# Kernel optimization log

Measured on AMD Instinct MI355X. Metric: run time of the kernel, lower is better.

Reference implementation:

```python
import jax, jax.numpy as jnp
import numpy as np

NUM_ROUTING_ITER = 3

def _squash(x):
    # Faithful to torch x.norm(): GLOBAL Frobenius norm over the whole tensor.
    n2 = jnp.sum(x * x)
    return x * (jnp.sqrt(n2) / (1.0 + n2))

def setup_inputs() -> dict:
    key = jax.random.key(0)
    k1, k2 = jax.random.split(key)
    x = jax.random.normal(k1, (256, 1152, 8), dtype=jnp.float32)
    weight = jax.random.normal(k2, (10, 1152, 8, 16), dtype=jnp.float32)
    return {"x": x, "weight": weight}

def reference(x, weight):
    # priors: [NC, B, IC, 1, OC] from [1,B,IC,1,L] @ [NC,1,IC,L,OC]
    priors = jnp.einsum('bil,nilo->nbio', x, weight)[:, :, :, None, :]
    b = jnp.zeros_like(priors)
    v = None
    for _ in range(NUM_ROUTING_ITER):
        # legacy F.softmax with no dim on a 5D tensor -> dim=1 (batch dim)
        c = jax.nn.softmax(b, axis=1)
        s = jnp.sum(c * priors, axis=2, keepdims=True)  # [NC,B,1,1,OC]
        v = _squash(s)
        b = b + jnp.sum(priors * v, axis=-1, keepdims=True)
    return v
```

## Files before the change

kernel.cpp:

```cpp
#include <hip/hip_runtime.h>
#include <math.h>

#define NC    10
#define BATCH 256
#define IC    1152
#define LDIM  8
#define OC    16

#define NCH   96
#define CH    (IC/NCH)
#define NBLK  (NC*NCH)
#define NTHR  256
#define NTOT  (NC*BATCH*OC)
#define NRED  160
#define KPG   (NCH/4)

typedef float f32x2 __attribute__((ext_vector_type(2)));

__device__ __forceinline__ void decode_nch(int bid, int& n, int& ch) {
    n = bid / NCH;
    int r = bid - n * NCH;
    ch = (r & 7) * (NCH / 8) + (r >> 3);
}

__device__ __forceinline__ float n2_reduce(const float* __restrict__ n2_part,
                                           float* redW, int t, int lane, int wid)
{
    float q = (t < NRED) ? n2_part[t] : 0.f;
#pragma unroll
    for (int m = 32; m >= 1; m >>= 1) q += __shfl_xor(q, m, 64);
    if (lane == 0) redW[wid] = q;
    __syncthreads();
    return redW[0] + redW[1] + redW[2] + redW[3];
}

__global__ __launch_bounds__(256) void k0_xT(const float* __restrict__ x,
                                             float* __restrict__ xT)
{
    int u = blockIdx.x * 256 + threadIdx.x;
    int i = u >> 9, r = u & 511, b = r >> 1, h = r & 1;
    reinterpret_cast<float4*>(xT)[u] =
        reinterpret_cast<const float4*>(x)[((size_t)b * IC + i) * 2 + h];
}

__global__ __launch_bounds__(256) void kA(
    const float* __restrict__ xT, const float* __restrict__ w,
    float* __restrict__ s_part)
{
    int n, ch; decode_nch(blockIdx.x, n, ch);
    int i0 = ch * CH;
    int t  = threadIdx.x;

    f32x2 sp2[8];
#pragma unroll
    for (int j = 0; j < 8; ++j) sp2[j] = (f32x2){0.f, 0.f};

    for (int ii = 0; ii < CH; ++ii) {
        int i = i0 + ii;
        const float4* xp = reinterpret_cast<const float4*>(xT)
                         + ((size_t)i * BATCH + t) * 2;
        float4 xa = xp[0], xb = xp[1];
        float xr[8] = {xa.x, xa.y, xa.z, xa.w, xb.x, xb.y, xb.z, xb.w};
        const f32x2* wp2 = reinterpret_cast<const f32x2*>(
            w + (size_t)__builtin_amdgcn_readfirstlane((n * IC + i) * (LDIM * OC)));
#pragma unroll
        for (int l = 0; l < LDIM; ++l) {
            f32x2 xl = {xr[l], xr[l]};
#pragma unroll
            for (int j = 0; j < 8; ++j)
                sp2[j] += wp2[l * 8 + j] * xl;
        }
    }
    float4* dst = reinterpret_cast<float4*>(s_part)
                + (((size_t)ch * NC + n) * BATCH + t) * 4;
    const float inv = 1.0f / 256.0f;
    dst[0] = make_float4(sp2[0].x*inv, sp2[0].y*inv, sp2[1].x*inv, sp2[1].y*inv);
    dst[1] = make_float4(sp2[2].x*inv, sp2[2].y*inv, sp2[3].x*inv, sp2[3].y*inv);
    dst[2] = make_float4(sp2[4].x*inv, sp2[4].y*inv, sp2[5].x*inv, sp2[5].y*inv);
    dst[3] = make_float4(sp2[6].x*inv, sp2[6].y*inv, sp2[7].x*inv, sp2[7].y*inv);
}

__global__ __launch_bounds__(256) void kR(const float* __restrict__ s_part,
                                          float* __restrict__ s,
                                          float* __restrict__ n2_part)
{
    __shared__ float4 lds[4][64];
    int t = threadIdx.x, lane = t & 63, g = t >> 6;
    int idx0 = blockIdx.x * 256;
    float4 a = make_float4(0.f, 0.f, 0.f, 0.f);
    for (int k = 0; k < KPG; ++k) {
        float4 v = *reinterpret_cast<const float4*>(
            s_part + (size_t)(g * KPG + k) * NTOT + idx0 + lane * 4);
        a.x += v.x; a.y += v.y; a.z += v.z; a.w += v.w;
    }
    lds[g][lane] = a;
    __syncthreads();
    if (t < 64) {
        float4 s0 = lds[0][t], s1 = lds[1][t], s2 = lds[2][t], s3 = lds[3][t];
        float4 sv = make_float4(s0.x+s1.x+s2.x+s3.x, s0.y+s1.y+s2.y+s3.y,
                                s0.z+s1.z+s2.z+s3.z, s0.w+s1.w+s2.w+s3.w);
        *reinterpret_cast<float4*>(s + idx0 + t * 4) = sv;
        float q = sv.x*sv.x + sv.y*sv.y + sv.z*sv.z + sv.w*sv.w;
#pragma unroll
        for (int m = 32; m >= 1; m >>= 1) q += __shfl_xor(q, m, 64);
        if (t == 0) n2_part[blockIdx.x] = q;
    }
}

template<bool FIRST>
__global__ __launch_bounds__(256) void kB(
    const float* __restrict__ xT, const float* __restrict__ w,
    const float* __restrict__ s, const float* __restrict__ n2_part,
    float* __restrict__ betaT, float* __restrict__ s_part)
{
    __shared__ float redA[2][4];
    __shared__ float redW[4];
    int t = threadIdx.x, lane = t & 63, wid = t >> 6;
    int n, ch; decode_nch(blockIdx.x, n, ch);
    int i0 = ch * CH;

    float n2 = n2_reduce(n2_part, redW, t, lane, wid);
    float sc = sqrtf(n2) / (1.0f + n2);

    f32x2 v2[8];
    {
        const f32x2* svp = reinterpret_cast<const f32x2*>(s)
                         + ((size_t)n * BATCH + t) * 8;
        f32x2 scv = {sc, sc};
#pragma unroll
        for (int j = 0; j < 8; ++j) v2[j] = svp[j] * scv;
    }

    f32x2 sp2[8];
#pragma unroll
    for (int j = 0; j < 8; ++j) sp2[j] = (f32x2){0.f, 0.f};

    const float4* xbase = reinterpret_cast<const float4*>(xT);
    size_t xo = ((size_t)i0 * BATCH + t) * 2;
    float4 xa = xbase[xo], xb = xbase[xo + 1];

    for (int ii = 0; ii < CH; ++ii) {
        int i = i0 + ii;
        float4 na = xa, nb = xb;
        if (ii + 1 < CH) {
            size_t nx = ((size_t)(i + 1) * BATCH + t) * 2;
            na = xbase[nx]; nb = xbase[nx + 1];
        }

        float xr[8] = {xa.x, xa.y, xa.z, xa.w, xb.x, xb.y, xb.z, xb.w};
        const f32x2* wp2 = reinterpret_cast<const f32x2*>(
            w + (size_t)__builtin_amdgcn_readfirstlane((n * IC + i) * (LDIM * OC)));

        f32x2 p2[8];
#pragma unroll
        for (int j = 0; j < 8; ++j) p2[j] = (f32x2){0.f, 0.f};
#pragma unroll
        for (int l = 0; l < LDIM; ++l) {
            f32x2 xl = {xr[l], xr[l]};
#pragma unroll
            for (int j = 0; j < 8; ++j)
                p2[j] += wp2[l * 8 + j] * xl;
        }

        f32x2 d2 = p2[0] * v2[0];
#pragma unroll
        for (int j = 1; j < 8; ++j) d2 += p2[j] * v2[j];
        float dot = d2.x + d2.y;

        size_t bidx = ((size_t)n * IC + i) * BATCH + t;
        float beta;
        if (FIRST) { beta = dot; betaT[bidx] = beta; }
        else       { beta = betaT[bidx] + dot; }

        float e = __expf(beta);
        float es = e;
#pragma unroll
        for (int m = 1; m < 64; m <<= 1) es += __shfl_xor(es, m, 64);
        if (lane == 0) redA[ii & 1][wid] = es;
        __syncthreads();
        float denom = redA[ii & 1][0] + redA[ii & 1][1]
                    + redA[ii & 1][2] + redA[ii & 1][3];
        float c = e * (1.0f / denom);
        f32x2 c2 = {c, c};
#pragma unroll
        for (int j = 0; j < 8; ++j) sp2[j] += c2 * p2[j];

        xa = na; xb = nb;
    }

    float4* dst = reinterpret_cast<float4*>(s_part)
                + (((size_t)ch * NC + n) * BATCH + t) * 4;
    dst[0] = make_float4(sp2[0].x, sp2[0].y, sp2[1].x, sp2[1].y);
    dst[1] = make_float4(sp2[2].x, sp2[2].y, sp2[3].x, sp2[3].y);
    dst[2] = make_float4(sp2[4].x, sp2[4].y, sp2[5].x, sp2[5].y);
    dst[3] = make_float4(sp2[6].x, sp2[6].y, sp2[7].x, sp2[7].y);
}

__global__ __launch_bounds__(256) void k_out(const float* __restrict__ s,
                                             const float* __restrict__ n2_part,
                                             float* __restrict__ out)
{
    __shared__ float redW[4];
    int t = threadIdx.x, lane = t & 63, wid = t >> 6;
    float n2 = n2_reduce(n2_part, redW, t, lane, wid);
    float sc = sqrtf(n2) / (1.0f + n2);
    int idx = blockIdx.x * 256 + t;
    out[idx] = s[idx] * sc;
}

extern "C" void kernel_launch(void* const* d_in, const int* in_sizes, int n_in,
                              void* d_out, int out_size, void* d_ws, size_t ws_size,
                              hipStream_t stream)
{
    const float* x = (const float*)d_in[0];
    const float* w = (const float*)d_in[1];
    float* out = (float*)d_out;
    float* ws  = (float*)d_ws;

    float* xT      = ws;
    float* betaT   = xT + (size_t)IC * BATCH * LDIM;
    float* s       = betaT + (size_t)NC * IC * BATCH;
    float* s_part  = s + (size_t)NC * BATCH * OC;
    float* n2_part = s_part + (size_t)NCH * NC * BATCH * OC;

    dim3 blk(256);

    k0_xT<<<2304, blk, 0, stream>>>(x, xT);
    kA<<<NBLK, blk, 0, stream>>>(xT, w, s_part);
    kR<<<NRED, blk, 0, stream>>>(s_part, s, n2_part);
    kB<true><<<NBLK, blk, 0, stream>>>(xT, w, s, n2_part, betaT, s_part);
    kR<<<NRED, blk, 0, stream>>>(s_part, s, n2_part);
    kB<false><<<NBLK, blk, 0, stream>>>(xT, w, s, n2_part, betaT, s_part);
    kR<<<NRED, blk, 0, stream>>>(s_part, s, n2_part);
    k_out<<<160, blk, 0, stream>>>(s, n2_part, out);
}
```

Measured before the change: 106.8 us.

## Process two capsule classes per block to reuse x loads and share barriers

kA and kB now handle a pair of output classes per block, so each x row is loaded once and used for two weight sets. This halves the x traffic and the number of per-iteration barriers relative to the work done, and block decoding now groups chunks by XCD. The grid shrinks to 480 blocks, which lowers occupancy and raises register pressure. The x prefetch in kB is dropped, and kR gains four independent accumulators to increase memory-level parallelism.

Result: slower. 134.2 us (+25.7%).

```diff
diff --git a/kernel.cpp b/kernel.cpp
--- a/kernel.cpp
+++ b/kernel.cpp
@@ -9,7 +9,8 @@
 
 #define NCH   96
 #define CH    (IC/NCH)
-#define NBLK  (NC*NCH)
+#define NPAIR 5
+#define NBLK  (NCH*NPAIR)
 #define NTHR  256
 #define NTOT  (NC*BATCH*OC)
 #define NRED  160
@@ -17,21 +18,10 @@
 
 typedef float f32x2 __attribute__((ext_vector_type(2)));
 
-__device__ __forceinline__ void decode_nch(int bid, int& n, int& ch) {
-    n = bid / NCH;
-    int r = bid - n * NCH;
-    ch = (r & 7) * (NCH / 8) + (r >> 3);
-}
-
-__device__ __forceinline__ float n2_reduce(const float* __restrict__ n2_part,
-                                           float* redW, int t, int lane, int wid)
-{
-    float q = (t < NRED) ? n2_part[t] : 0.f;
-#pragma unroll
-    for (int m = 32; m >= 1; m >>= 1) q += __shfl_xor(q, m, 64);
-    if (lane == 0) redW[wid] = q;
-    __syncthreads();
-    return redW[0] + redW[1] + redW[2] + redW[3];
+__device__ __forceinline__ void decode(int bid, int& ch, int& n0) {
+    int xcd = bid & 7, q = bid >> 3;
+    ch = xcd * 12 + (q % 12);
+    n0 = (q / 12) * 2;
 }
 
 __global__ __launch_bounds__(256) void k0_xT(const float* __restrict__ x,
@@ -47,13 +37,13 @@
     const float* __restrict__ xT, const float* __restrict__ w,
     float* __restrict__ s_part)
 {
-    int n, ch; decode_nch(blockIdx.x, n, ch);
+    int ch, n0; decode(blockIdx.x, ch, n0);
     int i0 = ch * CH;
     int t  = threadIdx.x;
 
-    f32x2 sp2[8];
-#pragma unroll
-    for (int j = 0; j < 8; ++j) sp2[j] = (f32x2){0.f, 0.f};
+    f32x2 spA[8], spB[8];
+#pragma unroll
+    for (int j = 0; j < 8; ++j) { spA[j] = (f32x2){0.f,0.f}; spB[j] = (f32x2){0.f,0.f}; }
 
     for (int ii = 0; ii < CH; ++ii) {
         int i = i0 + ii;
@@ -61,23 +51,30 @@
                          + ((size_t)i * BATCH + t) * 2;
         float4 xa = xp[0], xb = xp[1];
         float xr[8] = {xa.x, xa.y, xa.z, xa.w, xb.x, xb.y, xb.z, xb.w};
-        const f32x2* wp2 = reinterpret_cast<const f32x2*>(
-            w + (size_t)__builtin_amdgcn_readfirstlane((n * IC + i) * (LDIM * OC)));
+        const f32x2* w0 = reinterpret_cast<const f32x2*>(
+            w + (size_t)__builtin_amdgcn_readfirstlane((n0 * IC + i) * (LDIM * OC)));
+        const f32x2* w1 = reinterpret_cast<const f32x2*>(
+            w + (size_t)__builtin_amdgcn_readfirstlane(((n0+1) * IC + i) * (LDIM * OC)));
 #pragma unroll
         for (int l = 0; l < LDIM; ++l) {
             f32x2 xl = {xr[l], xr[l]};
 #pragma unroll
-            for (int j = 0; j < 8; ++j)
-                sp2[j] += wp2[l * 8 + j] * xl;
+            for (int j = 0; j < 8; ++j) {
+                spA[j] += w0[l * 8 + j] * xl;
+                spB[j] += w1[l * 8 + j] * xl;
+            }
         }
     }
-    float4* dst = reinterpret_cast<float4*>(s_part)
-                + (((size_t)ch * NC + n) * BATCH + t) * 4;
     const float inv = 1.0f / 256.0f;
-    dst[0] = make_float4(sp2[0].x*inv, sp2[0].y*inv, sp2[1].x*inv, sp2[1].y*inv);
-    dst[1] = make_float4(sp2[2].x*inv, sp2[2].y*inv, sp2[3].x*inv, sp2[3].y*inv);
-    dst[2] = make_float4(sp2[4].x*inv, sp2[4].y*inv, sp2[5].x*inv, sp2[5].y*inv);
-    dst[3] = make_float4(sp2[6].x*inv, sp2[6].y*inv, sp2[7].x*inv, sp2[7].y*inv);
+    float4* dA = reinterpret_cast<float4*>(s_part)
+               + (((size_t)ch * NC + n0) * BATCH + t) * 4;
+    float4* dB = reinterpret_cast<float4*>(s_part)
+               + (((size_t)ch * NC + n0 + 1) * BATCH + t) * 4;
+#pragma unroll
+    for (int j = 0; j < 4; ++j) {
+        dA[j] = make_float4(spA[2*j].x*inv, spA[2*j].y*inv, spA[2*j+1].x*inv, spA[2*j+1].y*inv);
+        dB[j] = make_float4(spB[2*j].x*inv, spB[2*j].y*inv, spB[2*j+1].x*inv, spB[2*j+1].y*inv);
+    }
 }
 
 __global__ __launch_bounds__(256) void kR(const float* __restrict__ s_part,
@@ -87,18 +84,26 @@
     __shared__ float4 lds[4][64];
     int t = threadIdx.x, lane = t & 63, g = t >> 6;
     int idx0 = blockIdx.x * 256;
-    float4 a = make_float4(0.f, 0.f, 0.f, 0.f);
-    for (int k = 0; k < KPG; ++k) {
-        float4 v = *reinterpret_cast<const float4*>(
-            s_part + (size_t)(g * KPG + k) * NTOT + idx0 + lane * 4);
-        a.x += v.x; a.y += v.y; a.z += v.z; a.w += v.w;
-    }
+    const float* base = s_part + idx0 + lane * 4;
+    float4 a0 = make_float4(0,0,0,0), a1 = a0, a2 = a0, a3 = a0;
+    for (int k = 0; k < KPG; k += 4) {
+        float4 v0 = *reinterpret_cast<const float4*>(base + (size_t)(g*KPG + k    ) * NTOT);
+        float4 v1 = *reinterpret_cast<const float4*>(base + (size_t)(g*KPG + k + 1) * NTOT);
+        float4 v2 = *reinterpret_cast<const float4*>(base + (size_t)(g*KPG + k + 2) * NTOT);
+        float4 v3 = *reinterpret_cast<const float4*>(base + (size_t)(g*KPG + k + 3) * NTOT);
+        a0.x += v0.x; a0.y += v0.y; a0.z += v0.z; a0.w += v0.w;
+        a1.x += v1.x; a1.y += v1.y; a1.z += v1.z; a1.w += v1.w;
+        a2.x += v2.x; a2.y += v2.y; a2.z += v2.z; a2.w += v2.w;
+        a3.x += v3.x; a3.y += v3.y; a3.z += v3.z; a3.w += v3.w;
+    }
+    float4 a = make_float4((a0.x+a1.x)+(a2.x+a3.x), (a0.y+a1.y)+(a2.y+a3.y),
+                           (a0.z+a1.z)+(a2.z+a3.z), (a0.w+a1.w)+(a2.w+a3.w));
     lds[g][lane] = a;
     __syncthreads();
     if (t < 64) {
         float4 s0 = lds[0][t], s1 = lds[1][t], s2 = lds[2][t], s3 = lds[3][t];
-        float4 sv = make_float4(s0.x+s1.x+s2.x+s3.x, s0.y+s1.y+s2.y+s3.y,
-                                s0.z+s1.z+s2.z+s3.z, s0.w+s1.w+s2.w+s3.w);
+        float4 sv = make_float4((s0.x+s1.x)+(s2.x+s3.x), (s0.y+s1.y)+(s2.y+s3.y),
+                                (s0.z+s1.z)+(s2.z+s3.z), (s0.w+s1.w)+(s2.w+s3.w));
         *reinterpret_cast<float4*>(s + idx0 + t * 4) = sv;
         float q = sv.x*sv.x + sv.y*sv.y + sv.z*sv.z + sv.w*sv.w;
 #pragma unroll
@@ -113,87 +118,100 @@
     const float* __restrict__ s, const float* __restrict__ n2_part,
     float* __restrict__ betaT, float* __restrict__ s_part)
 {
-    __shared__ float redA[2][4];
+    __shared__ float redA[2][2][4];
     __shared__ float redW[4];
     int t = threadIdx.x, lane = t & 63, wid = t >> 6;
-    int n, ch; decode_nch(blockIdx.x, n, ch);
+    int ch, n0; decode(blockIdx.x, ch, n0);
     int i0 = ch * CH;
 
-    float n2 = n2_reduce(n2_part, redW, t, lane, wid);
+    float q = (t < NRED) ? n2_part[t] : 0.f;
+#pragma unroll
+    for (int m = 32; m >= 1; m >>= 1) q += __shfl_xor(q, m, 64);
+    if (lane == 0) redW[wid] = q;
+    __syncthreads();
+    float n2 = (redW[0] + redW[1]) + (redW[2] + redW[3]);
     float sc = sqrtf(n2) / (1.0f + n2);
 
-    f32x2 v2[8];
+    f32x2 vA[8], vB[8];
     {
-        const f32x2* svp = reinterpret_cast<const f32x2*>(s)
-                         + ((size_t)n * BATCH + t) * 8;
         f32x2 scv = {sc, sc};
-#pragma unroll
-        for (int j = 0; j < 8; ++j) v2[j] = svp[j] * scv;
-    }
-
-    f32x2 sp2[8];
-#pragma unroll
-    for (int j = 0; j < 8; ++j) sp2[j] = (f32x2){0.f, 0.f};
-
-    const float4* xbase = reinterpret_cast<const float4*>(xT);
-    size_t xo = ((size_t)i0 * BATCH + t) * 2;
-    float4 xa = xbase[xo], xb = xbase[xo + 1];
+        const f32x2* sA = reinterpret_cast<const f32x2*>(s)
+                        + ((size_t)n0 * BATCH + t) * 8;
+        const f32x2* sB = reinterpret_cast<const f32x2*>(s)
+                        + ((size_t)(n0+1) * BATCH + t) * 8;
+#pragma unroll
+        for (int j = 0; j < 8; ++j) { vA[j] = sA[j] * scv; vB[j] = sB[j] * scv; }
+    }
+
+    f32x2 spA[8], spB[8];
+#pragma unroll
+    for (int j = 0; j < 8; ++j) { spA[j] = (f32x2){0.f,0.f}; spB[j] = (f32x2){0.f,0.f}; }
 
     for (int ii = 0; ii < CH; ++ii) {
         int i = i0 + ii;
-        float4 na = xa, nb = xb;
-        if (ii + 1 < CH) {
-            size_t nx = ((size_t)(i + 1) * BATCH + t) * 2;
-            na = xbase[nx]; nb = xbase[nx + 1];
-        }
-
+        const float4* xp = reinterpret_cast<const float4*>(xT)
+                         + ((size_t)i * BATCH + t) * 2;
+        float4 xa = xp[0], xb = xp[1];
         float xr[8] = {xa.x, xa.y, xa.z, xa.w, xb.x, xb.y, xb.z, xb.w};
-        const f32x2* wp2 = reinterpret_cast<const f32x2*>(
-            w + (size_t)__builtin_amdgcn_readfirstlane((n * IC + i) * (LDIM * OC)));
-
-        f32x2 p2[8];
-#pragma unroll
-        for (int j = 0; j < 8; ++j) p2[j] = (f32x2){0.f, 0.f};
+        const f32x2* w0 = reinterpret_cast<const f32x2*>(
+            w + (size_t)__builtin_amdgcn_readfirstlane((n0 * IC + i) * (LDIM * OC)));
+        const f32x2* w1 = reinterpret_cast<const f32x2*>(
+            w + (size_t)__builtin_amdgcn_readfirstlane(((n0+1) * IC + i) * (LDIM * OC)));
+
+        f32x2 pA[8], pB[8];
+#pragma unroll
+        for (int j = 0; j < 8; ++j) { pA[j] = (f32x2){0.f,0.f}; pB[j] = (f32x2){0.f,0.f}; }
 #pragma unroll
         for (int l = 0; l < LDIM; ++l) {
             f32x2 xl = {xr[l], xr[l]};
 #pragma unroll
-            for (int j = 0; j < 8; ++j)
-                p2[j] += wp2[l * 8 + j] * xl;
+            for (int j = 0; j < 8; ++j) {
+                pA[j] += w0[l * 8 + j] * xl;
+                pB[j] += w1[l * 8 + j] * xl;
+            }
         }
 
-        f32x2 d2 = p2[0] * v2[0];
-#pragma unroll
-        for (int j = 1; j < 8; ++j) d2 += p2[j] * v2[j];
-        float dot = d2.x + d2.y;
-
-        size_t bidx = ((size_t)n * IC + i) * BATCH + t;
-        float beta;
-        if (FIRST) { beta = dot; betaT[bidx] = beta; }
-        else       { beta = betaT[bidx] + dot; }
-
-        float e = __expf(beta);
-        float es = e;
-#pragma unroll
-        for (int m = 1; m < 64; m <<= 1) es += __shfl_xor(es, m, 64);
-        if (lane == 0) redA[ii & 1][wid] = es;
+        f32x2 dA = pA[0] * vA[0], dB = pB[0] * vB[0];
+#pragma unroll
+        for (int j = 1; j < 8; ++j) { dA += pA[j] * vA[j]; dB += pB[j] * vB[j]; }
+        float dotA = dA.x + dA.y, dotB = dB.x + dB.y;
+
+        size_t biA = ((size_t)n0 * IC + i) * BATCH + t;
+        size_t biB = ((size_t)(n0+1) * IC + i) * BATCH + t;
+        float betaA, betaB;
+        if (FIRST) { betaA = dotA; betaT[biA] = betaA;
+                     betaB = dotB; betaT[biB] = betaB; }
+        else       { betaA = betaT[biA] + dotA;
+                     betaB = betaT[biB] + dotB; }
+
+        float eA = __expf(betaA), eB = __expf(betaB);
+        float esA = eA, esB = eB;
+#pragma unroll
+        for (int m = 1; m < 64; m <<= 1) {
+            esA += __shfl_xor(esA, m, 64);
+            esB += __shfl_xor(esB, m, 64);
+        }
+        if (lane == 0) { redA[ii & 1][0][wid] = esA; redA[ii & 1][1][wid] = esB; }
         __syncthreads();
-        float denom = redA[ii & 1][0] + redA[ii & 1][1]
-                    + redA[ii & 1][2] + redA[ii & 1][3];
-        float c = e * (1.0f / denom);
-        f32x2 c2 = {c, c};
-#pragma unroll
-        for (int j = 0; j < 8; ++j) sp2[j] += c2 * p2[j];
-
-        xa = na; xb = nb;
-    }
-
-    float4* dst = reinterpret_cast<float4*>(s_part)
-                + (((size_t)ch * NC + n) * BATCH + t) * 4;
-    dst[0] = make_float4(sp2[0].x, sp2[0].y, sp2[1].x, sp2[1].y);
-    dst[1] = make_float4(sp2[2].x, sp2[2].y, sp2[3].x, sp2[3].y);
-    dst[2] = make_float4(sp2[4].x, sp2[4].y, sp2[5].x, sp2[5].y);
-    dst[3] = make_float4(sp2[6].x, sp2[6].y, sp2[7].x, sp2[7].y);
+        float denA = (redA[ii&1][0][0] + redA[ii&1][0][1])
+                   + (redA[ii&1][0][2] + redA[ii&1][0][3]);
+        float denB = (redA[ii&1][1][0] + redA[ii&1][1][1])
+                   + (redA[ii&1][1][2] + redA[ii&1][1][3]);
+        f32x2 cA = {eA / denA, eA / denA};
+        f32x2 cB = {eB / denB, eB / denB};
+#pragma unroll
+        for (int j = 0; j < 8; ++j) { spA[j] += cA * pA[j]; spB[j] += cB * pB[j]; }
+    }
+
+    float4* dA = reinterpret_cast<float4*>(s_part)
+               + (((size_t)ch * NC + n0) * BATCH + t) * 4;
+    float4* dB = reinterpret_cast<float4*>(s_part)
+               + (((size_t)ch * NC + n0 + 1) * BATCH + t) * 4;
+#pragma unroll
+    for (int j = 0; j < 4; ++j) {
+        dA[j] = make_float4(spA[2*j].x, spA[2*j].y, spA[2*j+1].x, spA[2*j+1].y);
+        dB[j] = make_float4(spB[2*j].x, spB[2*j].y, spB[2*j+1].x, spB[2*j+1].y);
+    }
 }
 
 __global__ __launch_bounds__(256) void k_out(const float* __restrict__ s,
@@ -202,7 +220,12 @@
 {
     __shared__ float redW[4];
     int t = threadIdx.x, lane = t & 63, wid = t >> 6;
-    float n2 = n2_reduce(n2_part, redW, t, lane, wid);
+    float q = (t < NRED) ? n2_part[t] : 0.f;
+#pragma unroll
+    for (int m = 32; m >= 1; m >>= 1) q += __shfl_xor(q, m, 64);
+    if (lane == 0) redW[wid] = q;
+    __syncthreads();
+    float n2 = (redW[0] + redW[1]) + (redW[2] + redW[3]);
     float sc = sqrtf(n2) / (1.0f + n2);
     int idx = blockIdx.x * 256 + t;
     out[idx] = s[idx] * sc;
@@ -220,8 +243,8 @@
     float* xT      = ws;
     float* betaT   = xT + (size_t)IC * BATCH * LDIM;
     float* s       = betaT + (size_t)NC * IC * BATCH;
-    float* s_part  = s + (size_t)NC * BATCH * OC;
-    float* n2_part = s_part + (size_t)NCH * NC * BATCH * OC;
+    float* s_part  = s + NTOT;
+    float* n2_part = s_part + (size_t)NCH * NTOT;
 
     dim3 blk(256);
 
@@ -232,5 +255,5 @@
     kR<<<NRED, blk, 0, stream>>>(s_part, s, n2_part);
     kB<false><<<NBLK, blk, 0, stream>>>(xT, w, s, n2_part, betaT, s_part);
     kR<<<NRED, blk, 0, stream>>>(s_part, s, n2_part);
-    k_out<<<160, blk, 0, stream>>>(s, n2_part, out);
-}
+    k_out<<<NRED, blk, 0, stream>>>(s, n2_part, out);
+}
```
